# Performance work log

Hardware: AMD Instinct MI355X
Metric: run time of the kernel (lower is better)

## Reference

```python
import jax, jax.numpy as jnp
import numpy as np

D_IN = 784
D = 768          # hidden_dim
R = 8            # num_rels
L = 3            # num_layers
B = 64           # graphs in batch
N = 32768        # total nodes
E = 262144       # total edges


def _layer_norm(x, g, b, eps=1e-5):
    m = x.mean(-1, keepdims=True)
    v = x.var(-1, keepdims=True)
    return (x - m) / jnp.sqrt(v + eps) * g + b


def setup_inputs() -> dict:
    key = jax.random.key(0)
    ks = jax.random.split(key, 24)
    s = 0.02
    inp = {
        "type_vec": jax.random.normal(ks[0], (N, 16), jnp.float32),
        "code_vec": jax.random.normal(ks[1], (N, D), jnp.float32),
        # input_proj: Linear(784,768) + LayerNorm(768)
        "W_in": jax.random.normal(ks[2], (D_IN, D), jnp.float32) * s,
        "b_in": jnp.zeros((D,), jnp.float32),
        "ln_in_g": jnp.ones((D,), jnp.float32),
        "ln_in_b": jnp.zeros((D,), jnp.float32),
        # RGCN layers (basis regularizer, num_bases=num_rels -> per-relation W)
        "W_rel": jax.random.normal(ks[3], (L, R, D, D), jnp.float32) * s,
        "W_loop": jax.random.normal(ks[4], (L, D, D), jnp.float32) * s,
        "rgcn_bias": jnp.zeros((L, D), jnp.float32),
        "ln_g": jnp.ones((L, D), jnp.float32),
        "ln_b": jnp.zeros((L, D), jnp.float32),
        # global attention pooling gate MLP: 768 -> 384 -> 1
        "Wg1": jax.random.normal(ks[5], (D, D // 2), jnp.float32) * s,
        "bg1": jnp.zeros((D // 2,), jnp.float32),
        "Wg2": jax.random.normal(ks[6], (D // 2, 1), jnp.float32) * s,
        "bg2": jnp.zeros((1,), jnp.float32),
        # classifier: 768 -> 512 (+LN) -> 2
        "Wc1": jax.random.normal(ks[7], (D, 512), jnp.float32) * s,
        "bc1": jnp.zeros((512,), jnp.float32),
        "ln_c_g": jnp.ones((512,), jnp.float32),
        "ln_c_b": jnp.zeros((512,), jnp.float32),
        "Wc2": jax.random.normal(ks[8], (512, 2), jnp.float32) * s,
        "bc2": jnp.zeros((2,), jnp.float32),
        # graph structure
        "src": jax.random.randint(ks[9], (E,), 0, N, jnp.int64),
        "dst": jax.random.randint(ks[10], (E,), 0, N, jnp.int64),
        "edge_type": jax.random.randint(ks[11], (E,), 0, R, jnp.int64),
        "node_graph": jnp.sort(jax.random.randint(ks[12], (N,), 0, B, jnp.int64)),
        "num_graphs": B,
    }
    return inp


def reference(type_vec, code_vec, W_in, b_in, ln_in_g, ln_in_b,
              W_rel, W_loop, rgcn_bias, ln_g, ln_b,
              Wg1, bg1, Wg2, bg2, Wc1, bc1, ln_c_g, ln_c_b, Wc2, bc2,
              src, dst, edge_type, node_graph, num_graphs):
    # input projection
    h = jnp.concatenate([type_vec, code_vec], axis=-1)           # [N, 784]
    h = jax.nn.gelu(_layer_norm(h @ W_in + b_in, ln_in_g, ln_in_b), approximate=False)
    n_nodes = h.shape[0]
    n_layers, n_rels = W_rel.shape[0], W_rel.shape[1]

    for l in range(n_layers):
        agg = jnp.zeros_like(h)
        for r in range(n_rels):
            # relation-specific transform, then gather->mask->scatter-add
            msg = (h @ W_rel[l, r])[src] * (edge_type == r).astype(h.dtype)[:, None]  # [E, D]
            agg = agg + jax.ops.segment_sum(msg, dst, num_segments=n_nodes)
        h_new = agg + rgcn_bias[l] + h @ W_loop[l]               # DGL: agg + bias + self-loop
        h = jax.nn.gelu(_layer_norm(h_new, ln_g[l], ln_b[l]), approximate=False)

    # global attention pooling (segment softmax over nodes of each graph)
    gate = (jax.nn.gelu(h @ Wg1 + bg1, approximate=False) @ Wg2 + bg2)[:, 0]  # [N]
    gmax = jax.ops.segment_max(gate, node_graph, num_segments=num_graphs)
    e = jnp.exp(gate - gmax[node_graph])
    denom = jax.ops.segment_sum(e, node_graph, num_segments=num_graphs)
    w = e / denom[node_graph]
    graph_repr = jax.ops.segment_sum(w[:, None] * h, node_graph, num_segments=num_graphs)  # [B, D]

    # classifier head
    z = jax.nn.gelu(_layer_norm(graph_repr @ Wc1 + bc1, ln_c_g, ln_c_b), approximate=False)
    logits = z @ Wc2 + bc2
    return jax.nn.log_softmax(logits, axis=-1)
```

## Files before the change

### kernel.cpp

```cpp
#include <hip/hip_runtime.h>
#include <hip/hip_bf16.h>

typedef __hip_bfloat16 bf16;
typedef __attribute__((ext_vector_type(8))) __bf16 bf16x8;
typedef __attribute__((ext_vector_type(4))) float f32x4;

#define N_NODES 32768
#define N_EDGES 262144
#define DIM 768
#define NGR 64
#define KIN 800
#define KSTACK 6912
#define NKEY (N_NODES * 8)

#define GLOBAL_AS __attribute__((address_space(1)))
#define LDS_AS __attribute__((address_space(3)))

__device__ __forceinline__ float gelu_f(float x) {
    return 0.5f * x * (1.0f + erff(x * 0.70710678118654752f));
}
__device__ __forceinline__ float bfu(unsigned short v) {
    union { unsigned u; float f; } x; x.u = (unsigned)v << 16; return x.f;
}
__device__ __forceinline__ unsigned short fbf(float f) {
    bf16 t = __float2bfloat16(f); return *(unsigned short*)&t;
}

__global__ __launch_bounds__(256)
void tcast_k(const float* __restrict__ in, bf16* __restrict__ out, int I, int O,
             int Ipad, int ostride) {
    __shared__ float t[32][33];
    const int i0 = blockIdx.x * 32, o0 = blockIdx.y * 32;
    const int tx = threadIdx.x & 31, ty = threadIdx.x >> 5;
#pragma unroll
    for (int q = 0; q < 4; ++q) {
        int i = i0 + ty + q * 8, o = o0 + tx;
        t[ty + q * 8][tx] = (i < I) ? in[(size_t)i * O + o] : 0.0f;
    }
    __syncthreads();
#pragma unroll
    for (int q = 0; q < 4; ++q) {
        int o = o0 + ty + q * 8, i = i0 + tx;
        if (i < Ipad) out[(size_t)o * ostride + i] = __float2bfloat16(t[tx][ty + q * 8]);
    }
}

__global__ __launch_bounds__(256)
void wprep_k(const float* __restrict__ W_rel, const float* __restrict__ W_loop,
             bf16* __restrict__ Wst) {
    __shared__ float t[32][33];
    const int z = blockIdx.z, l = z / 9, q = z % 9;
    const float* in = (q < 8) ? W_rel + ((size_t)(l * 8 + q)) * DIM * DIM
                              : W_loop + (size_t)l * DIM * DIM;
    bf16* out = Wst + (size_t)l * DIM * KSTACK + (q < 8 ? (q + 1) * DIM : 0);
    const int i0 = blockIdx.x * 32, o0 = blockIdx.y * 32;
    const int tx = threadIdx.x & 31, ty = threadIdx.x >> 5;
#pragma unroll
    for (int qq = 0; qq < 4; ++qq)
        t[ty + qq * 8][tx] = in[(size_t)(i0 + ty + qq * 8) * DIM + o0 + tx];
    __syncthreads();
#pragma unroll
    for (int qq = 0; qq < 4; ++qq)
        out[(size_t)(o0 + ty + qq * 8) * KSTACK + i0 + tx] =
            __float2bfloat16(t[tx][ty + qq * 8]);
}

__global__ __launch_bounds__(256)
void concat_k(const float* __restrict__ tv, const float* __restrict__ cv, bf16* __restrict__ X) {
    const int n = blockIdx.x;
    for (int c = threadIdx.x; c < KIN; c += 256) {
        float v = 0.0f;
        if (c < 16) v = tv[(size_t)n * 16 + c];
        else if (c < 784) v = cv[(size_t)n * DIM + (c - 16)];
        X[(size_t)n * KIN + c] = __float2bfloat16(v);
    }
}

__global__ __launch_bounds__(256)
void hist2_k(const int* __restrict__ dst, const int* __restrict__ et, int* __restrict__ deg) {
    int e = blockIdx.x * 256 + threadIdx.x;
    if (e < N_EDGES) atomicAdd(&deg[dst[e] * 8 + et[e]], 1);
}

__global__ __launch_bounds__(1024)
void scan2_k(const int* __restrict__ deg, int* __restrict__ rp, int* __restrict__ cur) {
    __shared__ int part[1024];
    const int t = threadIdx.x;
    const int base_i = t * 256;
    int s = 0;
    for (int i = 0; i < 256; ++i) s += deg[base_i + i];
    part[t] = s; __syncthreads();
    for (int st = 1; st < 1024; st <<= 1) {
        int v = (t >= st) ? part[t - st] : 0;
        __syncthreads();
        part[t] += v;
        __syncthreads();
    }
    int run = part[t] - s;
    for (int i = 0; i < 256; ++i) {
        int d = deg[base_i + i];
        rp[base_i + i] = run; cur[base_i + i] = run;
        run += d;
    }
    if (t == 1023) rp[NKEY] = run;
}

__global__ __launch_bounds__(256)
void place2_k(const int* __restrict__ src, const int* __restrict__ dst,
              const int* __restrict__ et, int* __restrict__ cur, int* __restrict__ eidx) {
    int e = blockIdx.x * 256 + threadIdx.x;
    if (e >= N_EDGES) return;
    int pos = atomicAdd(&cur[dst[e] * 8 + et[e]], 1);
    eidx[pos] = src[e];
}

template <int NC>
__global__ __launch_bounds__(256)
void gather2_k(const bf16* __restrict__ h, const int* __restrict__ rp2,
               const int* __restrict__ eidx, bf16* __restrict__ AGG, int rbase) {
    const int wave = threadIdx.x >> 6, lane = threadIdx.x & 63;
    const int n = blockIdx.x * 4 + wave;
    const int c0 = 2 * lane;
    unsigned short* outrow = (unsigned short*)&AGG[(size_t)n * (NC * DIM)];
    const int* bp = &rp2[n * 8 + rbase];
#pragma unroll 1
    for (int sel = 0; sel < NC; ++sel) {
        const int s = bp[sel], e = bp[sel + 1];
        float2 f[6] = {};
        for (int t = s; t < e; ++t) {
            const unsigned short* hs = (const unsigned short*)&h[(size_t)eidx[t] * DIM];
#pragma unroll
            for (int j = 0; j < 6; ++j) {
                ushort2 u = *(const ushort2*)&hs[c0 + j * 128];
                f[j].x += bfu(u.x); f[j].y += bfu(u.y);
            }
        }
#pragma unroll
        for (int j = 0; j < 6; ++j) {
            ushort2 o; o.x = fbf(f[j].x); o.y = fbf(f[j].y);
            *(ushort2*)&outrow[sel * DIM + c0 + j * 128] = o;
        }
    }
}

template <int ACCUM>
__global__ __launch_bounds__(512, 4)
void gemm256(const bf16* __restrict__ A1, int S1, int K1,
             const bf16* __restrict__ A2, int S2,
             const bf16* __restrict__ BT, int ldb,
             float* __restrict__ OUT, int Nn, int Ktot, int nbx) {
    __shared__ __align__(16) unsigned short lA[3][128 * 32];
    __shared__ __align__(16) unsigned short lB[3][256 * 32];
    const int nblk = gridDim.x;
    const int qx = nblk >> 3;
    const int bid = blockIdx.x;
    const int wgid = (bid & 7) * qx + (bid >> 3);
    const int bx = wgid % nbx, by = wgid / nbx;
    const int bn = bx * 256, bm = by * 128;
    const int tid = threadIdx.x;
    const int wave = tid >> 6, lane = tid & 63;
    const int wr = wave >> 2, wc = wave & 3;
    const int l15 = lane & 15, lg = lane >> 4;
    const int swz = (lg ^ (l15 >> 2)) * 8;

    f32x4 acc[4][4] = {};

    const int nt = Ktot >> 5;

    auto stage = [&](int t, int buf) {
        const int k0 = t * 32;
        const bf16* Ab; int koff, stA;
        if (k0 < K1) { Ab = A1; koff = k0; stA = S1; }
        else         { Ab = A2; koff = k0 - K1; stA = S2; }
        {
            const int row = tid >> 2, k8 = tid & 3;
            const int ks = k8 ^ ((row >> 2) & 3);
            const bf16* ga = Ab + (size_t)(bm + row) * stA + koff + ks * 8;
            __builtin_amdgcn_global_load_lds((const GLOBAL_AS void*)ga,
                (LDS_AS void*)&lA[buf][(wave * 64) * 8], 16, 0, 0);
        }
#pragma unroll
        for (int qq = 0; qq < 2; ++qq) {
            const int c = qq * 512 + tid;
            const int row = c >> 2, k8 = c & 3;
            const int ks = k8 ^ ((row >> 2) & 3);
            const bf16* gb = BT + (size_t)(bn + row) * ldb + k0 + ks * 8;
            __builtin_amdgcn_global_load_lds((const GLOBAL_AS void*)gb,
                (LDS_AS void*)&lB[buf][((qq * 8 + wave) * 64) * 8], 16, 0, 0);
        }
    };

    stage(0, 0);
    if (nt > 1) stage(1, 1);

    int rb = 0;
    for (int t = 0; t < nt; ++t) {
        if (t + 2 < nt) {
            int sb = rb + 2; if (sb >= 3) sb -= 3;
            stage(t + 2, sb);
            asm volatile("s_waitcnt vmcnt(6)" ::: "memory");
        } else if (t + 1 < nt) {
            asm volatile("s_waitcnt vmcnt(3)" ::: "memory");
        } else {
            asm volatile("s_waitcnt vmcnt(0)" ::: "memory");
        }
        __builtin_amdgcn_s_barrier();
        __builtin_amdgcn_sched_barrier(0);

        bf16x8 af[4], bfr[4];
#pragma unroll
        for (int mi = 0; mi < 4; ++mi) {
            const int r = wr * 64 + mi * 16 + l15;
            af[mi] = *reinterpret_cast<const bf16x8*>(&lA[rb][r * 32 + swz]);
        }
#pragma unroll
        for (int ni = 0; ni < 4; ++ni) {
            const int r = wc * 64 + ni * 16 + l15;
            bfr[ni] = *reinterpret_cast<const bf16x8*>(&lB[rb][r * 32 + swz]);
        }
        __builtin_amdgcn_s_setprio(1);
#pragma unroll
        for (int mi = 0; mi < 4; ++mi)
#pragma unroll
            for (int ni = 0; ni < 4; ++ni)
                acc[mi][ni] = __builtin_amdgcn_mfma_f32_16x16x32_bf16(af[mi], bfr[ni], acc[mi][ni], 0, 0, 0);
        __builtin_amdgcn_s_setprio(0);
        __builtin_amdgcn_sched_barrier(0);
        __builtin_amdgcn_s_barrier();

        rb = (rb == 2) ? 0 : rb + 1;
    }

#pragma unroll
    for (int mi = 0; mi < 4; ++mi)
#pragma unroll
        for (int ni = 0; ni < 4; ++ni) {
            const int r0 = bm + wr * 64 + mi * 16 + lg * 4;
            const int c0 = bn + wc * 64 + ni * 16 + l15;
#pragma unroll
            for (int i = 0; i < 4; ++i) {
                size_t idx = (size_t)(r0 + i) * Nn + c0;
                float v = acc[mi][ni][i];
                if (ACCUM) v += OUT[idx];
                OUT[idx] = v;
            }
        }
}

template <int ACCUM>
__global__ __launch_bounds__(256, 2)
void gemm_bt(const bf16* __restrict__ A1, int S1, int K1,
             const bf16* __restrict__ A2, int S2,
             const bf16* __restrict__ BT, int ldb,
             float* __restrict__ OUT, int Nn, int Ktot) {
    __shared__ __align__(16) unsigned short lA[128 * 32];
    __shared__ __align__(16) unsigned short lB[128 * 32];
    const int bn = blockIdx.x * 128;
    const int bm = blockIdx.y * 128;
    const int tid = threadIdx.x;
    const int wave = tid >> 6, lane = tid & 63;
    const int wr = wave >> 1, wc = wave & 1;
    const int l15 = lane & 15, lg = lane >> 4;

    f32x4 acc[4][4] = {};

    for (int k0 = 0; k0 < Ktot; k0 += 32) {
        const bf16* Ab; int koff, stA;
        if (k0 < K1) { Ab = A1; koff = k0; stA = S1; }
        else         { Ab = A2; koff = k0 - K1; stA = S2; }
#pragma unroll
        for (int q = 0; q < 2; ++q) {
            int c = wave * 128 + q * 64 + lane;
            int row = c >> 2, k8 = c & 3;
            const bf16* ga = Ab + (size_t)(bm + row) * stA + koff + k8 * 8;
            const bf16* gb = BT + (size_t)(bn + row) * ldb + k0 + k8 * 8;
            __builtin_amdgcn_global_load_lds((const GLOBAL_AS void*)ga,
                (LDS_AS void*)&lA[(wave * 128 + q * 64) * 8], 16, 0, 0);
            __builtin_amdgcn_global_load_lds((const GLOBAL_AS void*)gb,
                (LDS_AS void*)&lB[(wave * 128 + q * 64) * 8], 16, 0, 0);
        }
        __syncthreads();
        bf16x8 af[4], bfr[4];
#pragma unroll
        for (int mi = 0; mi < 4; ++mi)
            af[mi] = *reinterpret_cast<const bf16x8*>(&lA[(wr * 64 + mi * 16 + l15) * 32 + lg * 8]);
#pragma unroll
        for (int ni = 0; ni < 4; ++ni)
            bfr[ni] = *reinterpret_cast<const bf16x8*>(&lB[(wc * 64 + ni * 16 + l15) * 32 + lg * 8]);
#pragma unroll
        for (int mi = 0; mi < 4; ++mi)
#pragma unroll
            for (int ni = 0; ni < 4; ++ni)
                acc[mi][ni] = __builtin_amdgcn_mfma_f32_16x16x32_bf16(af[mi], bfr[ni], acc[mi][ni], 0, 0, 0);
        __syncthreads();
    }

#pragma unroll
    for (int mi = 0; mi < 4; ++mi)
#pragma unroll
        for (int ni = 0; ni < 4; ++ni) {
            const int r0 = bm + wr * 64 + mi * 16 + lg * 4;
            const int c0 = bn + wc * 64 + ni * 16 + l15;
#pragma unroll
            for (int i = 0; i < 4; ++i) {
                size_t idx = (size_t)(r0 + i) * Nn + c0;
                float v = acc[mi][ni][i];
                if (ACCUM) v += OUT[idx];
                OUT[idx] = v;
            }
        }
}

__global__ __launch_bounds__(256)
void ln_gelu_k(const float* __restrict__ ACC, const float* __restrict__ bias,
               const float* __restrict__ g, const float* __restrict__ b,
               bf16* __restrict__ hout) {
    const int wave = threadIdx.x >> 6, lane = threadIdx.x & 63;
    const int n = blockIdx.x * 4 + wave;
    float x[12];
    float s = 0.f, ss = 0.f;
#pragma unroll
    for (int j = 0; j < 12; ++j) {
        int c = lane + j * 64;
        x[j] = ACC[(size_t)n * DIM + c] + bias[c];
        s += x[j]; ss += x[j] * x[j];
    }
#pragma unroll
    for (int m = 1; m < 64; m <<= 1) { s += __shfl_xor(s, m, 64); ss += __shfl_xor(ss, m, 64); }
    const float mean = s * (1.f / DIM);
    const float var = ss * (1.f / DIM) - mean * mean;
    const float rstd = rsqrtf(var + 1e-5f);
#pragma unroll
    for (int j = 0; j < 12; ++j) {
        int c = lane + j * 64;
        float y = (x[j] - mean) * rstd * g[c] + b[c];
        hout[(size_t)n * DIM + c] = __float2bfloat16(gelu_f(y));
    }
}

__global__ __launch_bounds__(256)
void gate_k(const float* __restrict__ G1, const float* __restrict__ bg1,
            const float* __restrict__ Wg2, const float* __restrict__ bg2,
            float* __restrict__ gate) {
    const int wave = threadIdx.x >> 6, lane = threadIdx.x & 63;
    const int n = blockIdx.x * 4 + wave;
    float acc = 0.f;
#pragma unroll
    for (int j = 0; j < 6; ++j) {
        int c = lane + j * 64;
        float xv = G1[(size_t)n * 384 + c] + bg1[c];
        acc += gelu_f(xv) * Wg2[c];
    }
#pragma unroll
    for (int m = 1; m < 64; m <<= 1) acc += __shfl_xor(acc, m, 64);
    if (lane == 0) gate[n] = acc + bg2[0];
}

__device__ __forceinline__ int lower_bound_ng(const int* ng, int key) {
    int lo = 0, hi = N_NODES;
    while (lo < hi) { int mid = (lo + hi) >> 1; if (ng[mid] < key) lo = mid + 1; else hi = mid; }
    return lo;
}

__global__ __launch_bounds__(256)
void seg_stats_k(const float* __restrict__ gate, const int* __restrict__ ng,
                 float* __restrict__ gmax, float* __restrict__ gden) {
    __shared__ float red[256];
    const int b = blockIdx.x, t = threadIdx.x;
    const int start = lower_bound_ng(ng, b), end = lower_bound_ng(ng, b + 1);
    float m = -1e30f;
    for (int n = start + t; n < end; n += 256) m = fmaxf(m, gate[n]);
    red[t] = m; __syncthreads();
    for (int s = 128; s > 0; s >>= 1) { if (t < s) red[t] = fmaxf(red[t], red[t + s]); __syncthreads(); }
    const float gm = red[0]; __syncthreads();
    float ssum = 0.f;
    for (int n = start + t; n < end; n += 256) ssum += expf(gate[n] - gm);
    red[t] = ssum; __syncthreads();
    for (int s = 128; s > 0; s >>= 1) { if (t < s) red[t] += red[t + s]; __syncthreads(); }
    if (t == 0) { gmax[b] = gm; gden[b] = fmaxf(red[0], 1e-30f); }
}

__global__ __launch_bounds__(768)
void pool_k(const bf16* __restrict__ h, const float* __restrict__ gate,
            const int* __restrict__ ng, const float* __restrict__ gmax,
            const float* __restrict__ gden, float* __restrict__ grep) {
    const int b = blockIdx.x, c = threadIdx.x;
    const int start = lower_bound_ng(ng, b), end = lower_bound_ng(ng, b + 1);
    const float gm = gmax[b], inv = 1.0f / gden[b];
    const unsigned short* hv = (const unsigned short*)h;
    float a0 = 0.f, a1 = 0.f;
    int n = start;
    for (; n + 1 < end; n += 2) {
        float w0 = expf(gate[n] - gm) * inv;
        float w1 = expf(gate[n + 1] - gm) * inv;
        a0 += w0 * bfu(hv[(size_t)n * DIM + c]);
        a1 += w1 * bfu(hv[(size_t)(n + 1) * DIM + c]);
    }
    if (n < end) a0 += expf(gate[n] - gm) * inv * bfu(hv[(size_t)n * DIM + c]);
    grep[(size_t)b * DIM + c] = a0 + a1;
}

__global__ __launch_bounds__(512)
void cls_k(const float* __restrict__ grep, const float* __restrict__ Wc1,
           const float* __restrict__ bc1, const float* __restrict__ lng,
           const float* __restrict__ lnb, const float* __restrict__ Wc2,
           const float* __restrict__ bc2, float* __restrict__ out) {
    __shared__ float gr[DIM];
    __shared__ float red[512];
    const int b = blockIdx.x, j = threadIdx.x;
    for (int c = j; c < DIM; c += 512) gr[c] = grep[(size_t)b * DIM + c];
    __syncthreads();
    float a = bc1[j];
#pragma unroll 4
    for (int k = 0; k < DIM; ++k) a = fmaf(gr[k], Wc1[(size_t)k * 512 + j], a);
    red[j] = a; __syncthreads();
    for (int s = 256; s > 0; s >>= 1) { if (j < s) red[j] += red[j + s]; __syncthreads(); }
    const float mean = red[0] * (1.f / 512.f);
    __syncthreads();
    red[j] = (a - mean) * (a - mean); __syncthreads();
    for (int s = 256; s > 0; s >>= 1) { if (j < s) red[j] += red[j + s]; __syncthreads(); }
    const float rstd = rsqrtf(red[0] * (1.f / 512.f) + 1e-5f);
    __syncthreads();
    const float z = gelu_f((a - mean) * rstd * lng[j] + lnb[j]);
    red[j] = z * Wc2[2 * j + 0]; __syncthreads();
    for (int s = 256; s > 0; s >>= 1) { if (j < s) red[j] += red[j + s]; __syncthreads(); }
    const float l0 = red[0] + bc2[0];
    __syncthreads();
    red[j] = z * Wc2[2 * j + 1]; __syncthreads();
    for (int s = 256; s > 0; s >>= 1) { if (j < s) red[j] += red[j + s]; __syncthreads(); }
    if (j == 0) {
        const float l1 = red[0] + bc2[1];
        const float mx = fmaxf(l0, l1);
        const float lse = mx + logf(expf(l0 - mx) + expf(l1 - mx));
        out[2 * b + 0] = l0 - lse;
        out[2 * b + 1] = l1 - lse;
    }
}

extern "C" void kernel_launch(void* const* d_in, const int* in_sizes, int n_in,
                              void* d_out, int out_size, void* d_ws, size_t ws_size,
                              hipStream_t stream) {
    const float* type_vec = (const float*)d_in[0];
    const float* code_vec = (const float*)d_in[1];
    const float* W_in     = (const float*)d_in[2];
    const float* b_in     = (const float*)d_in[3];
    const float* ln_in_g  = (const float*)d_in[4];
    const float* ln_in_b  = (const float*)d_in[5];
    const float* W_rel    = (const float*)d_in[6];
    const float* W_loop   = (const float*)d_in[7];
    const float* rgcn_bias= (const float*)d_in[8];
    const float* ln_g     = (const float*)d_in[9];
    const float* ln_b     = (const float*)d_in[10];
    const float* Wg1      = (const float*)d_in[11];
    const float* bg1      = (const float*)d_in[12];
    const float* Wg2      = (const float*)d_in[13];
    const float* bg2      = (const float*)d_in[14];
    const float* Wc1      = (const float*)d_in[15];
    const float* bc1      = (const float*)d_in[16];
    const float* ln_c_g   = (const float*)d_in[17];
    const float* ln_c_b   = (const float*)d_in[18];
    const float* Wc2      = (const float*)d_in[19];
    const float* bc2      = (const float*)d_in[20];
    const int* src        = (const int*)d_in[21];
    const int* dst        = (const int*)d_in[22];
    const int* etype      = (const int*)d_in[23];
    const int* node_graph = (const int*)d_in[24];

    char* ws = (char*)d_ws;

    auto need = [](int nc) -> size_t {
        size_t base = 0;
        auto al = [&](size_t sz) { base = (base + sz + 255) & ~(size_t)255; };
        al((size_t)N_NODES * DIM * 2);
        al((size_t)N_NODES * DIM * 4);
        al((size_t)DIM * KIN * 2);
        al((size_t)3 * DIM * KSTACK * 2);
        al((size_t)384 * DIM * 2);
        size_t open = base;
        al((size_t)N_NODES * nc * DIM * 2);
        al((size_t)(NKEY + 1) * 4);
        al((size_t)NKEY * 4);
        al((size_t)NKEY * 4);
        al((size_t)N_EDGES * 4);
        al((size_t)N_NODES * 4);
        al(256); al(256);
        al((size_t)NGR * DIM * 4);
        size_t xend = open + (size_t)N_NODES * KIN * 2;
        return base > xend ? base : xend;
    };
    int nc = 1;
    if (ws_size >= need(4)) nc = 4;
    else if (ws_size >= need(2)) nc = 2;

    size_t off = 0;
    auto alloc = [&](size_t sz) { size_t r = off; off = (off + sz + 255) & ~(size_t)255; return r; };
    bf16*  h_bf  = (bf16*)(ws + alloc((size_t)N_NODES * DIM * 2));
    float* ACC   = (float*)(ws + alloc((size_t)N_NODES * DIM * 4));
    bf16*  WinT  = (bf16*)(ws + alloc((size_t)DIM * KIN * 2));
    bf16*  Wst   = (bf16*)(ws + alloc((size_t)3 * DIM * KSTACK * 2));
    bf16*  Wg1T  = (bf16*)(ws + alloc((size_t)384 * DIM * 2));
    size_t open  = off;
    bf16*  AGG   = (bf16*)(ws + alloc((size_t)N_NODES * nc * DIM * 2));
    int*   rp2   = (int*)(ws + alloc((size_t)(NKEY + 1) * 4));
    int*   cur2  = (int*)(ws + alloc((size_t)NKEY * 4));
    int*   deg2  = (int*)(ws + alloc((size_t)NKEY * 4));
    int*   eidx  = (int*)(ws + alloc((size_t)N_EDGES * 4));
    float* gate  = (float*)(ws + alloc((size_t)N_NODES * 4));
    float* gmax  = (float*)(ws + alloc(256));
    float* gden  = (float*)(ws + alloc(256));
    float* grep  = (float*)(ws + alloc((size_t)NGR * DIM * 4));
    bf16*  Xbf   = (bf16*)(ws + open);
    float* G1    = ACC;

    tcast_k<<<dim3(25, 24), 256, 0, stream>>>(W_in, WinT, 784, DIM, KIN, KIN);
    wprep_k<<<dim3(24, 24, 27), 256, 0, stream>>>(W_rel, W_loop, Wst);
    tcast_k<<<dim3(24, 12), 256, 0, stream>>>(Wg1, Wg1T, DIM, 384, DIM, DIM);

    concat_k<<<N_NODES, 256, 0, stream>>>(type_vec, code_vec, Xbf);
    gemm256<0><<<768, 512, 0, stream>>>(Xbf, KIN, KIN, Xbf, KIN, WinT, KIN, ACC, DIM, KIN, 3);
    ln_gelu_k<<<N_NODES / 4, 256, 0, stream>>>(ACC, b_in, ln_in_g, ln_in_b, h_bf);

    hipMemsetAsync(deg2, 0, (size_t)NKEY * 4, stream);
    hist2_k<<<N_EDGES / 256, 256, 0, stream>>>(dst, etype, deg2);
    scan2_k<<<1, 1024, 0, stream>>>(deg2, rp2, cur2);
    place2_k<<<N_EDGES / 256, 256, 0, stream>>>(src, dst, etype, cur2, eidx);

    const int nchunks = 8 / nc;
    for (int l = 0; l < 3; ++l) {
        bf16* Wl = Wst + (size_t)l * DIM * KSTACK;
        for (int c = 0; c < nchunks; ++c) {
            const int rbase = c * nc;
            if (nc == 1)      gather2_k<1><<<N_NODES / 4, 256, 0, stream>>>(h_bf, rp2, eidx, AGG, rbase);
            else if (nc == 2) gather2_k<2><<<N_NODES / 4, 256, 0, stream>>>(h_bf, rp2, eidx, AGG, rbase);
            else              gather2_k<4><<<N_NODES / 4, 256, 0, stream>>>(h_bf, rp2, eidx, AGG, rbase);
            if (c == 0) {
                gemm256<0><<<768, 512, 0, stream>>>(
                    h_bf, DIM, DIM, AGG, nc * DIM, Wl, KSTACK, ACC, DIM, DIM + nc * DIM, 3);
            } else {
                gemm256<1><<<768, 512, 0, stream>>>(
                    AGG, nc * DIM, nc * DIM, AGG, nc * DIM,
                    Wl + (size_t)DIM * (1 + rbase), KSTACK, ACC, DIM, nc * DIM, 3);
            }
        }
        ln_gelu_k<<<N_NODES / 4, 256, 0, stream>>>(ACC, rgcn_bias + l * DIM, ln_g + l * DIM,
                                                   ln_b + l * DIM, h_bf);
    }

    gemm_bt<0><<<dim3(3, 256), 256, 0, stream>>>(
        h_bf, DIM, DIM, h_bf, DIM, Wg1T, DIM, G1, 384, DIM);
    gate_k<<<N_NODES / 4, 256, 0, stream>>>(G1, bg1, Wg2, bg2, gate);
    seg_stats_k<<<NGR, 256, 0, stream>>>(gate, node_graph, gmax, gden);
    pool_k<<<NGR, 768, 0, stream>>>(h_bf, gate, node_graph, gmax, gden, grep);

    cls_k<<<NGR, 512, 0, stream>>>(grep, Wc1, bc1, ln_c_g, ln_c_b, Wc2, bc2, (float*)d_out);
}
```

Measured before the change: 2.686 ms.

## Shrink workspace to fit all 8 relations in one fused GEMM per layer

Reorganizes workspace so the aggregation buffer can hold all 8 relations, letting each layer run two gathers and a single K=6912 GEMM instead of chunked GEMMs with read-modify-write accumulation. To free space, the GEMM output accumulator becomes bf16, edge indices become 16-bit, and weight stacks are prepared per layer into one reused buffer. The LDS swizzle pattern also changes. Risks include bf16 accumulation precision loss, 16-bit source indices (N=32768 fits), and a fixed Wg1T offset inside AGG.

```diff
diff --git a/kernel.cpp b/kernel.cpp
--- a/kernel.cpp
+++ b/kernel.cpp
@@ -46,13 +46,12 @@
 }
 
 __global__ __launch_bounds__(256)
-void wprep_k(const float* __restrict__ W_rel, const float* __restrict__ W_loop,
-             bf16* __restrict__ Wst) {
+void wprep_l_k(const float* __restrict__ Wrel_l, const float* __restrict__ Wloop_l,
+               bf16* __restrict__ WstL) {
     __shared__ float t[32][33];
-    const int z = blockIdx.z, l = z / 9, q = z % 9;
-    const float* in = (q < 8) ? W_rel + ((size_t)(l * 8 + q)) * DIM * DIM
-                              : W_loop + (size_t)l * DIM * DIM;
-    bf16* out = Wst + (size_t)l * DIM * KSTACK + (q < 8 ? (q + 1) * DIM : 0);
+    const int q = blockIdx.z;
+    const float* in = (q < 8) ? Wrel_l + (size_t)q * DIM * DIM : Wloop_l;
+    bf16* out = WstL + (q < 8 ? (q + 1) * DIM : 0);
     const int i0 = blockIdx.x * 32, o0 = blockIdx.y * 32;
     const int tx = threadIdx.x & 31, ty = threadIdx.x >> 5;
 #pragma unroll
@@ -77,18 +76,18 @@
 }
 
 __global__ __launch_bounds__(256)
-void hist2_k(const int* __restrict__ dst, const int* __restrict__ et, int* __restrict__ deg) {
+void hist2_k(const int* __restrict__ dst, const int* __restrict__ et, int* __restrict__ cur) {
     int e = blockIdx.x * 256 + threadIdx.x;
-    if (e < N_EDGES) atomicAdd(&deg[dst[e] * 8 + et[e]], 1);
+    if (e < N_EDGES) atomicAdd(&cur[dst[e] * 8 + et[e]], 1);
 }
 
 __global__ __launch_bounds__(1024)
-void scan2_k(const int* __restrict__ deg, int* __restrict__ rp, int* __restrict__ cur) {
+void scan2_k(int* __restrict__ cur, int* __restrict__ rp) {
     __shared__ int part[1024];
     const int t = threadIdx.x;
     const int base_i = t * 256;
     int s = 0;
-    for (int i = 0; i < 256; ++i) s += deg[base_i + i];
+    for (int i = 0; i < 256; ++i) s += cur[base_i + i];
     part[t] = s; __syncthreads();
     for (int st = 1; st < 1024; st <<= 1) {
         int v = (t >= st) ? part[t - st] : 0;
@@ -98,7 +97,7 @@
     }
     int run = part[t] - s;
     for (int i = 0; i < 256; ++i) {
-        int d = deg[base_i + i];
+        int d = cur[base_i + i];
         rp[base_i + i] = run; cur[base_i + i] = run;
         run += d;
     }
@@ -107,21 +106,23 @@
 
 __global__ __launch_bounds__(256)
 void place2_k(const int* __restrict__ src, const int* __restrict__ dst,
-              const int* __restrict__ et, int* __restrict__ cur, int* __restrict__ eidx) {
+              const int* __restrict__ et, int* __restrict__ cur,
+              unsigned short* __restrict__ eidx) {
     int e = blockIdx.x * 256 + threadIdx.x;
     if (e >= N_EDGES) return;
     int pos = atomicAdd(&cur[dst[e] * 8 + et[e]], 1);
-    eidx[pos] = src[e];
+    eidx[pos] = (unsigned short)src[e];
 }
 
 template <int NC>
 __global__ __launch_bounds__(256)
 void gather2_k(const bf16* __restrict__ h, const int* __restrict__ rp2,
-               const int* __restrict__ eidx, bf16* __restrict__ AGG, int rbase) {
+               const unsigned short* __restrict__ eidx, bf16* __restrict__ AGG,
+               int rbase, int ostride, int colbase) {
     const int wave = threadIdx.x >> 6, lane = threadIdx.x & 63;
     const int n = blockIdx.x * 4 + wave;
     const int c0 = 2 * lane;
-    unsigned short* outrow = (unsigned short*)&AGG[(size_t)n * (NC * DIM)];
+    unsigned short* outrow = (unsigned short*)&AGG[(size_t)n * ostride + colbase];
     const int* bp = &rp2[n * 8 + rbase];
 #pragma unroll 1
     for (int sel = 0; sel < NC; ++sel) {
@@ -143,17 +144,15 @@
     }
 }
 
-template <int ACCUM>
+template <int MODE>
 __global__ __launch_bounds__(512, 4)
 void gemm256(const bf16* __restrict__ A1, int S1, int K1,
              const bf16* __restrict__ A2, int S2,
              const bf16* __restrict__ BT, int ldb,
-             float* __restrict__ OUT, int Nn, int Ktot, int nbx) {
+             bf16* __restrict__ OUT, int Nn, int Ktot, int nbx) {
     __shared__ __align__(16) unsigned short lA[3][128 * 32];
     __shared__ __align__(16) unsigned short lB[3][256 * 32];
-    const int nblk = gridDim.x;
-    const int qx = nblk >> 3;
-    const int bid = blockIdx.x;
+    const int nblk = gridDim.x, qx = nblk >> 3, bid = blockIdx.x;
     const int wgid = (bid & 7) * qx + (bid >> 3);
     const int bx = wgid % nbx, by = wgid / nbx;
     const int bn = bx * 256, bm = by * 128;
@@ -161,11 +160,10 @@
     const int wave = tid >> 6, lane = tid & 63;
     const int wr = wave >> 2, wc = wave & 3;
     const int l15 = lane & 15, lg = lane >> 4;
-    const int swz = (lg ^ (l15 >> 2)) * 8;
+    const int swz = (lg ^ ((l15 >> 1) & 3)) * 8;
 
     f32x4 acc[4][4] = {};
-
-    const int nt = Ktot >> 5;
+    const int nkt = Ktot >> 5;
 
     auto stage = [&](int t, int buf) {
         const int k0 = t * 32;
@@ -174,8 +172,8 @@
         else         { Ab = A2; koff = k0 - K1; stA = S2; }
         {
             const int row = tid >> 2, k8 = tid & 3;
-            const int ks = k8 ^ ((row >> 2) & 3);
-            const bf16* ga = Ab + (size_t)(bm + row) * stA + koff + ks * 8;
+            const int ks = (k8 ^ ((row >> 1) & 3)) * 8;
+            const bf16* ga = Ab + (size_t)(bm + row) * stA + koff + ks;
             __builtin_amdgcn_global_load_lds((const GLOBAL_AS void*)ga,
                 (LDS_AS void*)&lA[buf][(wave * 64) * 8], 16, 0, 0);
         }
@@ -183,23 +181,23 @@
         for (int qq = 0; qq < 2; ++qq) {
             const int c = qq * 512 + tid;
             const int row = c >> 2, k8 = c & 3;
-            const int ks = k8 ^ ((row >> 2) & 3);
-            const bf16* gb = BT + (size_t)(bn + row) * ldb + k0 + ks * 8;
+            const int ks = (k8 ^ ((row >> 1) & 3)) * 8;
+            const bf16* gb = BT + (size_t)(bn + row) * ldb + k0 + ks;
             __builtin_amdgcn_global_load_lds((const GLOBAL_AS void*)gb,
                 (LDS_AS void*)&lB[buf][((qq * 8 + wave) * 64) * 8], 16, 0, 0);
         }
     };
 
     stage(0, 0);
-    if (nt > 1) stage(1, 1);
+    if (nkt > 1) stage(1, 1);
 
     int rb = 0;
-    for (int t = 0; t < nt; ++t) {
-        if (t + 2 < nt) {
+    for (int t = 0; t < nkt; ++t) {
+        if (t + 2 < nkt) {
             int sb = rb + 2; if (sb >= 3) sb -= 3;
             stage(t + 2, sb);
             asm volatile("s_waitcnt vmcnt(6)" ::: "memory");
-        } else if (t + 1 < nt) {
+        } else if (t + 1 < nkt) {
             asm volatile("s_waitcnt vmcnt(3)" ::: "memory");
         } else {
             asm volatile("s_waitcnt vmcnt(0)" ::: "memory");
@@ -231,6 +229,7 @@
         rb = (rb == 2) ? 0 : rb + 1;
     }
 
+    unsigned short* O = (unsigned short*)OUT;
 #pragma unroll
     for (int mi = 0; mi < 4; ++mi)
 #pragma unroll
@@ -241,16 +240,14 @@
             for (int i = 0; i < 4; ++i) {
                 size_t idx = (size_t)(r0 + i) * Nn + c0;
                 float v = acc[mi][ni][i];
-                if (ACCUM) v += OUT[idx];
-                OUT[idx] = v;
+                if (MODE == 1) v += bfu(O[idx]);
+                O[idx] = fbf(v);
             }
         }
 }
 
-template <int ACCUM>
 __global__ __launch_bounds__(256, 2)
-void gemm_bt(const bf16* __restrict__ A1, int S1, int K1,
-             const bf16* __restrict__ A2, int S2,
+void gemm_bt(const bf16* __restrict__ A1, int S1,
              const bf16* __restrict__ BT, int ldb,
              float* __restrict__ OUT, int Nn, int Ktot) {
     __shared__ __align__(16) unsigned short lA[128 * 32];
@@ -265,14 +262,11 @@
     f32x4 acc[4][4] = {};
 
     for (int k0 = 0; k0 < Ktot; k0 += 32) {
-        const bf16* Ab; int koff, stA;
-        if (k0 < K1) { Ab = A1; koff = k0; stA = S1; }
-        else         { Ab = A2; koff = k0 - K1; stA = S2; }
 #pragma unroll
         for (int q = 0; q < 2; ++q) {
             int c = wave * 128 + q * 64 + lane;
             int row = c >> 2, k8 = c & 3;
-            const bf16* ga = Ab + (size_t)(bm + row) * stA + koff + k8 * 8;
+            const bf16* ga = A1 + (size_t)(bm + row) * S1 + k0 + k8 * 8;
             const bf16* gb = BT + (size_t)(bn + row) * ldb + k0 + k8 * 8;
             __builtin_amdgcn_global_load_lds((const GLOBAL_AS void*)ga,
                 (LDS_AS void*)&lA[(wave * 128 + q * 64) * 8], 16, 0, 0);
@@ -302,27 +296,24 @@
             const int r0 = bm + wr * 64 + mi * 16 + lg * 4;
             const int c0 = bn + wc * 64 + ni * 16 + l15;
 #pragma unroll
-            for (int i = 0; i < 4; ++i) {
-                size_t idx = (size_t)(r0 + i) * Nn + c0;
-                float v = acc[mi][ni][i];
-                if (ACCUM) v += OUT[idx];
-                OUT[idx] = v;
-            }
-        }
-}
-
-__global__ __launch_bounds__(256)
-void ln_gelu_k(const float* __restrict__ ACC, const float* __restrict__ bias,
+            for (int i = 0; i < 4; ++i)
+                OUT[(size_t)(r0 + i) * Nn + c0] = acc[mi][ni][i];
+        }
+}
+
+__global__ __launch_bounds__(256)
+void ln_gelu_k(const bf16* __restrict__ ACCb, const float* __restrict__ bias,
                const float* __restrict__ g, const float* __restrict__ b,
                bf16* __restrict__ hout) {
     const int wave = threadIdx.x >> 6, lane = threadIdx.x & 63;
     const int n = blockIdx.x * 4 + wave;
+    const unsigned short* Ab = (const unsigned short*)ACCb;
     float x[12];
     float s = 0.f, ss = 0.f;
 #pragma unroll
     for (int j = 0; j < 12; ++j) {
         int c = lane + j * 64;
-        x[j] = ACC[(size_t)n * DIM + c] + bias[c];
+        x[j] = bfu(Ab[(size_t)n * DIM + c]) + bias[c];
         s += x[j]; ss += x[j] * x[j];
     }
 #pragma unroll
@@ -468,86 +459,81 @@
 
     char* ws = (char*)d_ws;
 
-    auto need = [](int nc) -> size_t {
-        size_t base = 0;
-        auto al = [&](size_t sz) { base = (base + sz + 255) & ~(size_t)255; };
-        al((size_t)N_NODES * DIM * 2);
-        al((size_t)N_NODES * DIM * 4);
-        al((size_t)DIM * KIN * 2);
-        al((size_t)3 * DIM * KSTACK * 2);
-        al((size_t)384 * DIM * 2);
-        size_t open = base;
-        al((size_t)N_NODES * nc * DIM * 2);
-        al((size_t)(NKEY + 1) * 4);
-        al((size_t)NKEY * 4);
-        al((size_t)NKEY * 4);
-        al((size_t)N_EDGES * 4);
-        al((size_t)N_NODES * 4);
-        al(256); al(256);
-        al((size_t)NGR * DIM * 4);
-        size_t xend = open + (size_t)N_NODES * KIN * 2;
-        return base > xend ? base : xend;
+    auto lay = [&](int nc, bool doAssign,
+                   bf16*& h_bf, bf16*& ACCb, bf16*& WstL, int*& rp2, int*& cur2,
+                   unsigned short*& eidx, float*& gate, float*& gmax, float*& gden,
+                   float*& grep, bf16*& AGG) -> size_t {
+        size_t off = 0;
+        auto alloc = [&](size_t sz) { size_t r = off; off = (off + sz + 255) & ~(size_t)255; return r; };
+        size_t oH   = alloc((size_t)N_NODES * DIM * 2);
+        size_t oAC  = alloc((size_t)N_NODES * DIM * 2);
+        size_t oWL  = alloc((size_t)DIM * KSTACK * 2);
+        size_t oRP  = alloc((size_t)(NKEY + 1) * 4);
+        size_t oCU  = alloc((size_t)NKEY * 4);
+        size_t oEI  = alloc((size_t)N_EDGES * 2);
+        size_t oGA  = alloc((size_t)N_NODES * 4);
+        size_t oGM  = alloc(256);
+        size_t oGD  = alloc(256);
+        size_t oGR  = alloc((size_t)NGR * DIM * 4);
+        size_t oAG  = alloc((size_t)N_NODES * nc * DIM * 2);
+        if (doAssign) {
+            h_bf = (bf16*)(ws + oH);   ACCb = (bf16*)(ws + oAC);
+            WstL = (bf16*)(ws + oWL);  rp2  = (int*)(ws + oRP);
+            cur2 = (int*)(ws + oCU);   eidx = (unsigned short*)(ws + oEI);
+            gate = (float*)(ws + oGA); gmax = (float*)(ws + oGM);
+            gden = (float*)(ws + oGD); grep = (float*)(ws + oGR);
+            AGG  = (bf16*)(ws + oAG);
+        }
+        return off;
     };
-    int nc = 1;
-    if (ws_size >= need(4)) nc = 4;
-    else if (ws_size >= need(2)) nc = 2;
-
-    size_t off = 0;
-    auto alloc = [&](size_t sz) { size_t r = off; off = (off + sz + 255) & ~(size_t)255; return r; };
-    bf16*  h_bf  = (bf16*)(ws + alloc((size_t)N_NODES * DIM * 2));
-    float* ACC   = (float*)(ws + alloc((size_t)N_NODES * DIM * 4));
-    bf16*  WinT  = (bf16*)(ws + alloc((size_t)DIM * KIN * 2));
-    bf16*  Wst   = (bf16*)(ws + alloc((size_t)3 * DIM * KSTACK * 2));
-    bf16*  Wg1T  = (bf16*)(ws + alloc((size_t)384 * DIM * 2));
-    size_t open  = off;
-    bf16*  AGG   = (bf16*)(ws + alloc((size_t)N_NODES * nc * DIM * 2));
-    int*   rp2   = (int*)(ws + alloc((size_t)(NKEY + 1) * 4));
-    int*   cur2  = (int*)(ws + alloc((size_t)NKEY * 4));
-    int*   deg2  = (int*)(ws + alloc((size_t)NKEY * 4));
-    int*   eidx  = (int*)(ws + alloc((size_t)N_EDGES * 4));
-    float* gate  = (float*)(ws + alloc((size_t)N_NODES * 4));
-    float* gmax  = (float*)(ws + alloc(256));
-    float* gden  = (float*)(ws + alloc(256));
-    float* grep  = (float*)(ws + alloc((size_t)NGR * DIM * 4));
-    bf16*  Xbf   = (bf16*)(ws + open);
-    float* G1    = ACC;
+
+    bf16 *h_bf, *ACCb, *WstL, *AGG; int *rp2, *cur2; unsigned short* eidx;
+    float *gate, *gmax, *gden, *grep;
+    bf16 *d0=nullptr,*d1=nullptr,*d2=nullptr,*d3=nullptr; int *d4=nullptr,*d5=nullptr;
+    unsigned short* d6=nullptr; float *d7=nullptr,*d8=nullptr,*d9=nullptr,*d10=nullptr;
+    const bool big = ws_size >= lay(8, false, d0,d1,d2,d4,d5,d6,d7,d8,d9,d10,d3);
+    const int nc = big ? 8 : 4;
+    lay(nc, true, h_bf, ACCb, WstL, rp2, cur2, eidx, gate, gmax, gden, grep, AGG);
+
+    bf16* Xbf  = AGG;
+    bf16* WinT = (bf16*)((char*)AGG + (size_t)N_NODES * KIN * 2);
+    float* G1  = (float*)AGG;
+
+    const int AGW = nc * DIM;
 
     tcast_k<<<dim3(25, 24), 256, 0, stream>>>(W_in, WinT, 784, DIM, KIN, KIN);
-    wprep_k<<<dim3(24, 24, 27), 256, 0, stream>>>(W_rel, W_loop, Wst);
+    concat_k<<<N_NODES, 256, 0, stream>>>(type_vec, code_vec, Xbf);
+    gemm256<0><<<768, 512, 0, stream>>>(Xbf, KIN, KIN, Xbf, KIN, WinT, KIN, ACCb, DIM, KIN, 3);
+    ln_gelu_k<<<N_NODES / 4, 256, 0, stream>>>(ACCb, b_in, ln_in_g, ln_in_b, h_bf);
+
+    hipMemsetAsync(cur2, 0, (size_t)NKEY * 4, stream);
+    hist2_k<<<N_EDGES / 256, 256, 0, stream>>>(dst, etype, cur2);
+    scan2_k<<<1, 1024, 0, stream>>>(cur2, rp2);
+    place2_k<<<N_EDGES / 256, 256, 0, stream>>>(src, dst, etype, cur2, eidx);
+
+    for (int l = 0; l < 3; ++l) {
+        wprep_l_k<<<dim3(24, 24, 9), 256, 0, stream>>>(
+            W_rel + (size_t)l * 8 * DIM * DIM, W_loop + (size_t)l * DIM * DIM, WstL);
+        if (nc == 8) {
+            gather2_k<4><<<N_NODES / 4, 256, 0, stream>>>(h_bf, rp2, eidx, AGG, 0, AGW, 0);
+            gather2_k<4><<<N_NODES / 4, 256, 0, stream>>>(h_bf, rp2, eidx, AGG, 4, AGW, 4 * DIM);
+            gemm256<0><<<768, 512, 0, stream>>>(
+                h_bf, DIM, DIM, AGG, AGW, WstL, KSTACK, ACCb, DIM, KSTACK, 3);
+        } else {
+            gather2_k<4><<<N_NODES / 4, 256, 0, stream>>>(h_bf, rp2, eidx, AGG, 0, AGW, 0);
+            gemm256<0><<<768, 512, 0, stream>>>(
+                h_bf, DIM, DIM, AGG, AGW, WstL, KSTACK, ACCb, DIM, DIM + 4 * DIM, 3);
+            gather2_k<4><<<N_NODES / 4, 256, 0, stream>>>(h_bf, rp2, eidx, AGG, 4, AGW, 0);
+            gemm256<1><<<768, 512, 0, stream>>>(
+                AGG, AGW, AGW, AGG, AGW, WstL + (size_t)DIM * 5, KSTACK, ACCb, DIM, 4 * DIM, 3);
+        }
+        ln_gelu_k<<<N_NODES / 4, 256, 0, stream>>>(ACCb, rgcn_bias + l * DIM, ln_g + l * DIM,
+                                                   ln_b + l * DIM, h_bf);
+    }
+
+    bf16* Wg1T = (bf16*)((char*)AGG + 60 * 1024 * 1024);
     tcast_k<<<dim3(24, 12), 256, 0, stream>>>(Wg1, Wg1T, DIM, 384, DIM, DIM);
-
-    concat_k<<<N_NODES, 256, 0, stream>>>(type_vec, code_vec, Xbf);
-    gemm256<0><<<768, 512, 0, stream>>>(Xbf, KIN, KIN, Xbf, KIN, WinT, KIN, ACC, DIM, KIN, 3);
-    ln_gelu_k<<<N_NODES / 4, 256, 0, stream>>>(ACC, b_in, ln_in_g, ln_in_b, h_bf);
-
-    hipMemsetAsync(deg2, 0, (size_t)NKEY * 4, stream);
-    hist2_k<<<N_EDGES / 256, 256, 0, stream>>>(dst, etype, deg2);
-    scan2_k<<<1, 1024, 0, stream>>>(deg2, rp2, cur2);
-    place2_k<<<N_EDGES / 256, 256, 0, stream>>>(src, dst, etype, cur2, eidx);
-
-    const int nchunks = 8 / nc;
-    for (int l = 0; l < 3; ++l) {
-        bf16* Wl = Wst + (size_t)l * DIM * KSTACK;
-        for (int c = 0; c < nchunks; ++c) {
-            const int rbase = c * nc;
-            if (nc == 1)      gather2_k<1><<<N_NODES / 4, 256, 0, stream>>>(h_bf, rp2, eidx, AGG, rbase);
-            else if (nc == 2) gather2_k<2><<<N_NODES / 4, 256, 0, stream>>>(h_bf, rp2, eidx, AGG, rbase);
-            else              gather2_k<4><<<N_NODES / 4, 256, 0, stream>>>(h_bf, rp2, eidx, AGG, rbase);
-            if (c == 0) {
-                gemm256<0><<<768, 512, 0, stream>>>(
-                    h_bf, DIM, DIM, AGG, nc * DIM, Wl, KSTACK, ACC, DIM, DIM + nc * DIM, 3);
-            } else {
-                gemm256<1><<<768, 512, 0, stream>>>(
-                    AGG, nc * DIM, nc * DIM, AGG, nc * DIM,
-                    Wl + (size_t)DIM * (1 + rbase), KSTACK, ACC, DIM, nc * DIM, 3);
-            }
-        }
-        ln_gelu_k<<<N_NODES / 4, 256, 0, stream>>>(ACC, rgcn_bias + l * DIM, ln_g + l * DIM,
-                                                   ln_b + l * DIM, h_bf);
-    }
-
-    gemm_bt<0><<<dim3(3, 256), 256, 0, stream>>>(
-        h_bf, DIM, DIM, h_bf, DIM, Wg1T, DIM, G1, 384, DIM);
+    gemm_bt<<<dim3(3, 256), 256, 0, stream>>>(h_bf, DIM, Wg1T, DIM, G1, 384, DIM);
     gate_k<<<N_NODES / 4, 256, 0, stream>>>(G1, bg1, Wg2, bg2, gate);
     seg_stats_k<<<NGR, 256, 0, stream>>>(gate, node_graph, gmax, gden);
     pool_k<<<NGR, 768, 0, stream>>>(h_bf, gate, node_graph, gmax, gden, grep);
```

Result: faster. 2.492 ms (-7.2%).
